# Optimization experiments

Measured on AMD Instinct MI355X. Metric: run time of the kernel, lower is better.

## Reference

```python
import jax, jax.numpy as jnp
import numpy as np

N = 50000       # num nodes
E = 800000      # num edges
F_NODE = 64     # node feature dim
F_EDGE = 16     # edge feature dim
HID = 32        # hidden_channels (per head)
HEADS = 4
HC = HEADS * HID  # 128
COND = 128      # condition_dim
NEG = 0.2       # GATv2 leaky_relu slope


def _lin(k, fi, fo):
    kw, kb = jax.random.split(k)
    s = 1.0 / np.sqrt(fi)
    W = jax.random.uniform(kw, (fi, fo), minval=-s, maxval=s, dtype=jnp.float32)
    b = jax.random.uniform(kb, (fo,), minval=-s, maxval=s, dtype=jnp.float32)
    return W, b


def setup_inputs() -> dict:
    key = jax.random.key(0)
    ks = jax.random.split(key, 16)
    x = jax.random.normal(ks[0], (N, F_NODE), dtype=jnp.float32)
    edge_index = jax.random.randint(ks[1], (2, E), 0, N)
    edge_attr = jax.random.normal(ks[2], (1, E, F_EDGE), dtype=jnp.float32)
    # conv1 params (GATv2Conv: lin_l, lin_r, lin_edge(no bias), att, out bias)
    w1l, b1l = _lin(ks[3], F_NODE, HC)
    w1r, b1r = _lin(ks[4], F_NODE, HC)
    w1e, _ = _lin(ks[5], F_EDGE, HC)
    att1 = jax.random.normal(ks[6], (HEADS, HID), dtype=jnp.float32) * 0.1
    bias1 = jnp.zeros((HC,), jnp.float32)
    # conv2 params
    w2l, b2l = _lin(ks[7], HC, HC)
    w2r, b2r = _lin(ks[8], HC, HC)
    w2e, _ = _lin(ks[9], F_EDGE, HC)
    att2 = jax.random.normal(ks[10], (HEADS, HID), dtype=jnp.float32) * 0.1
    bias2 = jnp.zeros((HC,), jnp.float32)
    # history_encoder
    hw, hb = _lin(ks[11], HC, COND)
    return dict(x=x, edge_index=edge_index, edge_attr=edge_attr,
                w1l=w1l, b1l=b1l, w1r=w1r, b1r=b1r, w1e=w1e, att1=att1, bias1=bias1,
                w2l=w2l, b2l=b2l, w2r=w2r, b2r=b2r, w2e=w2e, att2=att2, bias2=bias2,
                hw=hw, hb=hb)


def _gatv2(x, src, tgt, eattr, Wl, bl, Wr, br, We, att, bout):
    # x: [N, Fin]; src/tgt: [Ef]; eattr: [Ef, F_EDGE]
    xl = (x @ Wl + bl).reshape(-1, HEADS, HID)   # source transform
    xr = (x @ Wr + br).reshape(-1, HEADS, HID)   # target transform
    ee = (eattr @ We).reshape(-1, HEADS, HID)
    m = jax.nn.leaky_relu(xl[src] + xr[tgt] + ee, NEG)   # [Ef, H, C]
    logit = jnp.einsum('ehc,hc->eh', m, att)             # [Ef, H]
    # numerically-stable edge softmax over each target node's neighborhood
    mx = jax.ops.segment_max(logit, tgt, num_segments=N)
    p = jnp.exp(logit - mx[tgt])
    den = jax.ops.segment_sum(p, tgt, num_segments=N)
    alpha = p / den[tgt]                                 # [Ef, H]
    out = jax.ops.segment_sum(xl[src] * alpha[..., None], tgt, num_segments=N)
    return out.reshape(-1, HC) + bout                    # concat heads + bias


def reference(x, edge_index, edge_attr,
              w1l, b1l, w1r, b1r, w1e, att1, bias1,
              w2l, b2l, w2r, b2r, w2e, att2, bias2,
              hw, hb):
    ea = edge_attr[0]                      # edge_attr.squeeze(0)
    src, tgt = edge_index[0], edge_index[1]
    # add_self_loops with fill_value='mean': per-target mean of incoming edge_attr
    cnt = jax.ops.segment_sum(jnp.ones((E,), jnp.float32), tgt, num_segments=N)
    loop_attr = jax.ops.segment_sum(ea, tgt, num_segments=N) / jnp.maximum(cnt, 1.0)[:, None]
    loops = jnp.arange(N)
    src_f = jnp.concatenate([src, loops])
    tgt_f = jnp.concatenate([tgt, loops])
    ea_f = jnp.concatenate([ea, loop_attr], axis=0)
    h = jax.nn.relu(_gatv2(x, src_f, tgt_f, ea_f, w1l, b1l, w1r, b1r, w1e, att1, bias1))
    h = jax.nn.relu(_gatv2(h, src_f, tgt_f, ea_f, w2l, b2l, w2r, b2r, w2e, att2, bias2))
    h = h[None]                            # repeat to batch = edge_attr.size(0) = 1
    c = h @ hw + hb                        # history_encoder -> [1, N, COND]
    return c
```

## Files before the change

### kernel.cpp

```cpp
#include <hip/hip_runtime.h>
#include <hip/hip_bf16.h>
#include <math.h>

#define N_NODES 50000
#define N_EDGES 800000
#define NEG     0.2f

#define OFF_CNT    0
#define OFF_ROWPTR 50000
#define OFF_CURSOR 100000
#define OFF_PART   150000
#define OFF_CSRSE  150256
#define OFF_XL     1750272
#define OFF_XR     8150272

#define SCAN_BLOCKS 196
#define LNT 8

__global__ void hist_cnt_kernel(const int* __restrict__ tgt, int* __restrict__ cnt)
{
    int e = blockIdx.x * 256 + threadIdx.x;
    if (e >= N_EDGES) return;
    atomicAdd(&cnt[tgt[e]], 1);
}

__global__ void scanA_kernel(const int* __restrict__ cnt, int* __restrict__ rowptr,
                             int* __restrict__ part)
{
    __shared__ int s[256];
    int tid = threadIdx.x;
    int g = blockIdx.x * 256 + tid;
    int v = (g < N_NODES) ? cnt[g] : 0;
    s[tid] = v;
    __syncthreads();
    for (int off = 1; off < 256; off <<= 1) {
        int t = (tid >= off) ? s[tid - off] : 0;
        __syncthreads();
        s[tid] += t;
        __syncthreads();
    }
    if (g < N_NODES) rowptr[g] = s[tid] - v;
    if (tid == 255) part[blockIdx.x] = s[255];
}

__global__ void scanB_kernel(int* __restrict__ part)
{
    __shared__ int s[256];
    int tid = threadIdx.x;
    int v = (tid < SCAN_BLOCKS) ? part[tid] : 0;
    s[tid] = v;
    __syncthreads();
    for (int off = 1; off < 256; off <<= 1) {
        int t = (tid >= off) ? s[tid - off] : 0;
        __syncthreads();
        s[tid] += t;
        __syncthreads();
    }
    part[tid] = s[tid] - v;
}

__global__ void scanC_kernel(int* __restrict__ rowptr, const int* __restrict__ part,
                             int* __restrict__ cursor)
{
    int g = blockIdx.x * 256 + threadIdx.x;
    if (g >= N_NODES) return;
    int r = rowptr[g] + part[blockIdx.x];
    rowptr[g] = r;
    cursor[g] = r;
}

__global__ void scatter_kernel(const int* __restrict__ src, const int* __restrict__ tgt,
                               int* __restrict__ cursor, int2* __restrict__ csr_se)
{
    int e = blockIdx.x * 256 + threadIdx.x;
    if (e >= N_EDGES) return;
    int pos = atomicAdd(&cursor[tgt[e]], 1);
    csr_se[pos] = make_int2(src[e], e);
}

template<int K>
__global__ __launch_bounds__(128) void lin_kernel(const float* __restrict__ X,
    const float* __restrict__ Wl, const float* __restrict__ bl,
    const float* __restrict__ Wr, const float* __restrict__ br,
    float* __restrict__ xl, float* __restrict__ xr)
{
    __shared__ float s[LNT][K];
    int j = threadIdx.x;
    int nb = blockIdx.x * LNT;
    for (int t = 0; t < LNT; ++t) {
        int n = nb + t;
        if (n < N_NODES)
            for (int k = j; k < K; k += 128) s[t][k] = X[(size_t)n * K + k];
    }
    __syncthreads();
    float accL[LNT], accR[LNT];
    float blj = bl[j], brj = br[j];
    #pragma unroll
    for (int t = 0; t < LNT; ++t) { accL[t] = blj; accR[t] = brj; }
    for (int k = 0; k < K; ++k) {
        float wl = Wl[k * 128 + j], wr = Wr[k * 128 + j];
        #pragma unroll
        for (int t = 0; t < LNT; ++t) {
            accL[t] = fmaf(s[t][k], wl, accL[t]);
            accR[t] = fmaf(s[t][k], wr, accR[t]);
        }
    }
    for (int t = 0; t < LNT; ++t) {
        int n = nb + t;
        if (n < N_NODES) {
            xl[(size_t)n * 128 + j] = accL[t];
            xr[(size_t)n * 128 + j] = accR[t];
        }
    }
}

__global__ __launch_bounds__(256) void fused_kernel(
    const float* __restrict__ xl, const float* __restrict__ xr,
    const float* __restrict__ ea,
    const int2* __restrict__ csr_se, const int* __restrict__ rowptr,
    const int* __restrict__ cnt,
    const float* __restrict__ We, const float* __restrict__ att,
    const float* __restrict__ bias, float* __restrict__ out)
{
    __shared__ __align__(64) float sEa[4][4][16];
    int tid = threadIdx.x;
    int wave = tid >> 6, lane = tid & 63;
    int n = blockIdx.x * 4 + wave;
    if (n >= N_NODES) return;
    int c0 = lane * 2;
    int slot = lane >> 4, feat = lane & 15;

    float wreg0[16], wreg1[16];
    #pragma unroll
    for (int k = 0; k < 16; ++k) {
        float2 w2 = *(const float2*)(We + k * 128 + c0);
        wreg0[k] = w2.x; wreg1[k] = w2.y;
    }
    float a0 = att[c0], a1 = att[c0 + 1];

    int base = rowptr[n];
    int deg  = cnt[n];
    float2 xrt = *(const float2*)(xr + (size_t)n * 128 + c0);
    float2 xln = *(const float2*)(xl + (size_t)n * 128 + c0);

    float m = -INFINITY, den = 0.f, acc0 = 0.f, acc1 = 0.f;
    float eesum0 = 0.f, eesum1 = 0.f;

    int2 nse0 = make_int2(0, 0), nse1 = nse0, nse2 = nse0, nse3 = nse0;
    if (deg > 0) {
        nse0 = csr_se[base];     nse1 = csr_se[base + 1];
        nse2 = csr_se[base + 2]; nse3 = csr_se[base + 3];
    }
    for (int i = 0; i < deg; i += 4) {
        int2 se0 = nse0, se1 = nse1, se2 = nse2, se3 = nse3;
        bool v1 = (i + 1) < deg, v2 = (i + 2) < deg, v3 = (i + 3) < deg;
        int s0 = se0.x,           e0 = se0.y;
        int s1 = v1 ? se1.x : s0, e1 = v1 ? se1.y : e0;
        int s2 = v2 ? se2.x : s0, e2 = v2 ? se2.y : e0;
        int s3 = v3 ? se3.x : s0, e3 = v3 ? se3.y : e0;

        int es = (slot == 0) ? e0 : ((slot == 1) ? e1 : ((slot == 2) ? e2 : e3));
        sEa[wave][slot][feat] = ea[(size_t)es * 16 + feat];

        float2 x0 = *(const float2*)(xl + (size_t)s0 * 128 + c0);
        float2 x1 = *(const float2*)(xl + (size_t)s1 * 128 + c0);
        float2 x2 = *(const float2*)(xl + (size_t)s2 * 128 + c0);
        float2 x3 = *(const float2*)(xl + (size_t)s3 * 128 + c0);

        if (i + 4 < deg) {
            nse0 = csr_se[base + i + 4]; nse1 = csr_se[base + i + 5];
            nse2 = csr_se[base + i + 6]; nse3 = csr_se[base + i + 7];
        }

        float p0, p1, p2, p3;
#define EDGE_BODY(J, XJ, PJ, VJ)                                              \
        {                                                                     \
            const float4* er4 = (const float4*)&sEa[wave][J][0];              \
            float4 f0 = er4[0], f1 = er4[1], f2 = er4[2], f3 = er4[3];        \
            float t0 = f0.x * wreg0[0], t1 = f0.x * wreg1[0];                 \
            t0 = fmaf(f0.y, wreg0[1], t0);  t1 = fmaf(f0.y, wreg1[1], t1);    \
            t0 = fmaf(f0.z, wreg0[2], t0);  t1 = fmaf(f0.z, wreg1[2], t1);    \
            t0 = fmaf(f0.w, wreg0[3], t0);  t1 = fmaf(f0.w, wreg1[3], t1);    \
            t0 = fmaf(f1.x, wreg0[4], t0);  t1 = fmaf(f1.x, wreg1[4], t1);    \
            t0 = fmaf(f1.y, wreg0[5], t0);  t1 = fmaf(f1.y, wreg1[5], t1);    \
            t0 = fmaf(f1.z, wreg0[6], t0);  t1 = fmaf(f1.z, wreg1[6], t1);    \
            t0 = fmaf(f1.w, wreg0[7], t0);  t1 = fmaf(f1.w, wreg1[7], t1);    \
            t0 = fmaf(f2.x, wreg0[8], t0);  t1 = fmaf(f2.x, wreg1[8], t1);    \
            t0 = fmaf(f2.y, wreg0[9], t0);  t1 = fmaf(f2.y, wreg1[9], t1);    \
            t0 = fmaf(f2.z, wreg0[10], t0); t1 = fmaf(f2.z, wreg1[10], t1);   \
            t0 = fmaf(f2.w, wreg0[11], t0); t1 = fmaf(f2.w, wreg1[11], t1);   \
            t0 = fmaf(f3.x, wreg0[12], t0); t1 = fmaf(f3.x, wreg1[12], t1);   \
            t0 = fmaf(f3.y, wreg0[13], t0); t1 = fmaf(f3.y, wreg1[13], t1);   \
            t0 = fmaf(f3.z, wreg0[14], t0); t1 = fmaf(f3.z, wreg1[14], t1);   \
            t0 = fmaf(f3.w, wreg0[15], t0); t1 = fmaf(f3.w, wreg1[15], t1);   \
            eesum0 += (VJ) ? t0 : 0.f;      eesum1 += (VJ) ? t1 : 0.f;        \
            float q0 = XJ.x + xrt.x + t0;   q0 = (q0 > 0.f) ? q0 : NEG * q0;  \
            float q1 = XJ.y + xrt.y + t1;   q1 = (q1 > 0.f) ? q1 : NEG * q1;  \
            PJ = fmaf(q0, a0, q1 * a1);                                       \
        }
        EDGE_BODY(0, x0, p0, true)
        EDGE_BODY(1, x1, p1, v1)
        EDGE_BODY(2, x2, p2, v2)
        EDGE_BODY(3, x3, p3, v3)
#undef EDGE_BODY

        #pragma unroll
        for (int msk = 1; msk < 16; msk <<= 1) {
            p0 += __shfl_xor(p0, msk);
            p1 += __shfl_xor(p1, msk);
            p2 += __shfl_xor(p2, msk);
            p3 += __shfl_xor(p3, msk);
        }
        p1 = v1 ? p1 : -INFINITY;
        p2 = v2 ? p2 : -INFINITY;
        p3 = v3 ? p3 : -INFINITY;

        float nm = fmaxf(fmaxf(m, p0), fmaxf(fmaxf(p1, p2), p3));
        float sc = __expf(m - nm);
        float w0 = __expf(p0 - nm), w1 = __expf(p1 - nm);
        float w2 = __expf(p2 - nm), w3 = __expf(p3 - nm);
        den  = fmaf(den, sc, (w0 + w1) + (w2 + w3));
        acc0 = fmaf(acc0, sc, fmaf(w0, x0.x, fmaf(w1, x1.x, fmaf(w2, x2.x, w3 * x3.x))));
        acc1 = fmaf(acc1, sc, fmaf(w0, x0.y, fmaf(w1, x1.y, fmaf(w2, x2.y, w3 * x3.y))));
        m = nm;
    }

    {
        float rc = 1.0f / (float)(deg > 0 ? deg : 1);
        float ee0 = eesum0 * rc, ee1 = eesum1 * rc;
        float q0 = xln.x + xrt.x + ee0; q0 = (q0 > 0.f) ? q0 : NEG * q0;
        float q1 = xln.y + xrt.y + ee1; q1 = (q1 > 0.f) ? q1 : NEG * q1;
        float part = fmaf(q0, a0, q1 * a1);
        part += __shfl_xor(part, 1);
        part += __shfl_xor(part, 2);
        part += __shfl_xor(part, 4);
        part += __shfl_xor(part, 8);
        float nm = fmaxf(m, part);
        float sc = __expf(m - nm);
        float w  = __expf(part - nm);
        den  = fmaf(den, sc, w);
        acc0 = fmaf(acc0, sc, w * xln.x);
        acc1 = fmaf(acc1, sc, w * xln.y);
    }
    float rd = 1.0f / den;
    float o0 = fmaxf(fmaf(acc0, rd, bias[c0]), 0.f);
    float o1 = fmaxf(fmaf(acc1, rd, bias[c0 + 1]), 0.f);
    *(float2*)(out + (size_t)n * 128 + c0) = make_float2(o0, o1);
}

__global__ __launch_bounds__(128) void hist_kernel(float* __restrict__ io,
    const float* __restrict__ hw, const float* __restrict__ hb)
{
    __shared__ float s[LNT][128];
    int j = threadIdx.x;
    int nb = blockIdx.x * LNT;
    for (int t = 0; t < LNT; ++t) {
        int n = nb + t;
        if (n < N_NODES) s[t][j] = io[(size_t)n * 128 + j];
    }
    __syncthreads();
    float acc[LNT];
    float b = hb[j];
    #pragma unroll
    for (int t = 0; t < LNT; ++t) acc[t] = b;
    for (int k = 0; k < 128; ++k) {
        float w = hw[k * 128 + j];
        #pragma unroll
        for (int t = 0; t < LNT; ++t) acc[t] = fmaf(s[t][k], w, acc[t]);
    }
    for (int t = 0; t < LNT; ++t) {
        int n = nb + t;
        if (n < N_NODES) io[(size_t)n * 128 + j] = acc[t];
    }
}

extern "C" void kernel_launch(void* const* d_in, const int* in_sizes, int n_in,
                              void* d_out, int out_size, void* d_ws, size_t ws_size,
                              hipStream_t stream)
{
    const float* x    = (const float*)d_in[0];
    const int*   ei   = (const int*)d_in[1];
    const float* ea   = (const float*)d_in[2];
    const float* w1l  = (const float*)d_in[3];
    const float* b1l  = (const float*)d_in[4];
    const float* w1r  = (const float*)d_in[5];
    const float* b1r  = (const float*)d_in[6];
    const float* w1e  = (const float*)d_in[7];
    const float* att1 = (const float*)d_in[8];
    const float* bias1= (const float*)d_in[9];
    const float* w2l  = (const float*)d_in[10];
    const float* b2l  = (const float*)d_in[11];
    const float* w2r  = (const float*)d_in[12];
    const float* b2r  = (const float*)d_in[13];
    const float* w2e  = (const float*)d_in[14];
    const float* att2 = (const float*)d_in[15];
    const float* bias2= (const float*)d_in[16];
    const float* hw   = (const float*)d_in[17];
    const float* hb   = (const float*)d_in[18];
    const int* src = ei;
    const int* tgt = ei + N_EDGES;

    float* ws     = (float*)d_ws;
    int*   cnt    = (int*)(ws + OFF_CNT);
    int*   rowptr = (int*)(ws + OFF_ROWPTR);
    int*   cursor = (int*)(ws + OFF_CURSOR);
    int*   part   = (int*)(ws + OFF_PART);
    int2*  csr_se = (int2*)(ws + OFF_CSRSE);
    float* xl     = ws + OFF_XL;
    float* xr     = ws + OFF_XR;
    float* out    = (float*)d_out;

    hipMemsetAsync(cnt, 0, (size_t)N_NODES * 4, stream);

    hist_cnt_kernel<<<(N_EDGES + 255) / 256, 256, 0, stream>>>(tgt, cnt);
    scanA_kernel<<<SCAN_BLOCKS, 256, 0, stream>>>(cnt, rowptr, part);
    scanB_kernel<<<1, 256, 0, stream>>>(part);
    scanC_kernel<<<SCAN_BLOCKS, 256, 0, stream>>>(rowptr, part, cursor);
    scatter_kernel<<<(N_EDGES + 255) / 256, 256, 0, stream>>>(src, tgt, cursor, csr_se);

    lin_kernel<64><<<N_NODES / LNT, 128, 0, stream>>>(x, w1l, b1l, w1r, b1r, xl, xr);
    fused_kernel<<<(N_NODES + 3) / 4, 256, 0, stream>>>(
        xl, xr, ea, csr_se, rowptr, cnt, w1e, att1, bias1, out);

    lin_kernel<128><<<N_NODES / LNT, 128, 0, stream>>>(out, w2l, b2l, w2r, b2r, xl, xr);
    fused_kernel<<<(N_NODES + 3) / 4, 256, 0, stream>>>(
        xl, xr, ea, csr_se, rowptr, cnt, w2e, att2, bias2, out);

    hist_kernel<<<N_NODES / LNT, 128, 0, stream>>>(out, hw, hb);
}
```

Baseline: 659.1 us.

## Replace node linear kernels with register-tiled shared-memory GEMM

The per-layer lin kernels and the history-encoder kernel are replaced by one templated GEMM. It stages the whole weight matrix in LDS and computes 4x4 output tiles per thread with float4 loads, looping over 32-row tiles in a persistent grid of 1024 blocks. The aim is to stop re-reading weights from global memory for every small 8-node block and to raise arithmetic intensity. In exchange, the left and right projections are now separate launches that each read X again. The K=128 variant uses about 80KB of LDS per block, which may limit occupancy.

```diff
diff --git a/kernel.cpp b/kernel.cpp
--- a/kernel.cpp
+++ b/kernel.cpp
@@ -15,7 +15,6 @@
 #define OFF_XR     8150272
 
 #define SCAN_BLOCKS 196
-#define LNT 8
 
 __global__ void hist_cnt_kernel(const int* __restrict__ tgt, int* __restrict__ cnt)
 {
@@ -78,39 +77,50 @@
     csr_se[pos] = make_int2(src[e], e);
 }
 
-template<int K>
-__global__ __launch_bounds__(128) void lin_kernel(const float* __restrict__ X,
-    const float* __restrict__ Wl, const float* __restrict__ bl,
-    const float* __restrict__ Wr, const float* __restrict__ br,
-    float* __restrict__ xl, float* __restrict__ xr)
-{
-    __shared__ float s[LNT][K];
-    int j = threadIdx.x;
-    int nb = blockIdx.x * LNT;
-    for (int t = 0; t < LNT; ++t) {
-        int n = nb + t;
-        if (n < N_NODES)
-            for (int k = j; k < K; k += 128) s[t][k] = X[(size_t)n * K + k];
-    }
-    __syncthreads();
-    float accL[LNT], accR[LNT];
-    float blj = bl[j], brj = br[j];
-    #pragma unroll
-    for (int t = 0; t < LNT; ++t) { accL[t] = blj; accR[t] = brj; }
-    for (int k = 0; k < K; ++k) {
-        float wl = Wl[k * 128 + j], wr = Wr[k * 128 + j];
-        #pragma unroll
-        for (int t = 0; t < LNT; ++t) {
-            accL[t] = fmaf(s[t][k], wl, accL[t]);
-            accR[t] = fmaf(s[t][k], wr, accR[t]);
-        }
-    }
-    for (int t = 0; t < LNT; ++t) {
-        int n = nb + t;
-        if (n < N_NODES) {
-            xl[(size_t)n * 128 + j] = accL[t];
-            xr[(size_t)n * 128 + j] = accR[t];
-        }
+template<int KK>
+__global__ __launch_bounds__(256) void gemm_kernel(
+    const float* __restrict__ X, const float* __restrict__ W,
+    const float* __restrict__ bias, float* __restrict__ Y)
+{
+    __shared__ float sW[KK * 128];
+    __shared__ float sX[32 * KK];
+    int tid = threadIdx.x;
+    for (int idx = tid * 4; idx < KK * 128; idx += 1024)
+        *(float4*)&sW[idx] = *(const float4*)&W[idx];
+    int tc = (tid & 31) * 4;
+    int tn = (tid >> 5) * 4;
+    float4 b4 = *(const float4*)&bias[tc];
+
+    for (int tb = blockIdx.x * 32; tb < N_NODES; tb += gridDim.x * 32) {
+        __syncthreads();
+        for (int idx = tid * 4; idx < 32 * KK; idx += 1024) {
+            if (tb + idx / KK < N_NODES)
+                *(float4*)&sX[idx] = *(const float4*)&X[(size_t)tb * KK + idx];
+        }
+        __syncthreads();
+        float4 a0 = b4, a1 = b4, a2 = b4, a3 = b4;
+#define FMA4(A, S, Wv) A.x = fmaf(S, Wv.x, A.x); A.y = fmaf(S, Wv.y, A.y); \
+                       A.z = fmaf(S, Wv.z, A.z); A.w = fmaf(S, Wv.w, A.w);
+        for (int k = 0; k < KK; k += 4) {
+            float4 x0 = *(const float4*)&sX[(tn + 0) * KK + k];
+            float4 x1 = *(const float4*)&sX[(tn + 1) * KK + k];
+            float4 x2 = *(const float4*)&sX[(tn + 2) * KK + k];
+            float4 x3 = *(const float4*)&sX[(tn + 3) * KK + k];
+            float4 w0 = *(const float4*)&sW[(k + 0) * 128 + tc];
+            float4 w1 = *(const float4*)&sW[(k + 1) * 128 + tc];
+            float4 w2 = *(const float4*)&sW[(k + 2) * 128 + tc];
+            float4 w3 = *(const float4*)&sW[(k + 3) * 128 + tc];
+            FMA4(a0, x0.x, w0) FMA4(a0, x0.y, w1) FMA4(a0, x0.z, w2) FMA4(a0, x0.w, w3)
+            FMA4(a1, x1.x, w0) FMA4(a1, x1.y, w1) FMA4(a1, x1.z, w2) FMA4(a1, x1.w, w3)
+            FMA4(a2, x2.x, w0) FMA4(a2, x2.y, w1) FMA4(a2, x2.z, w2) FMA4(a2, x2.w, w3)
+            FMA4(a3, x3.x, w0) FMA4(a3, x3.y, w1) FMA4(a3, x3.z, w2) FMA4(a3, x3.w, w3)
+        }
+#undef FMA4
+        int n0 = tb + tn;
+        if (n0 + 0 < N_NODES) *(float4*)&Y[(size_t)(n0 + 0) * 128 + tc] = a0;
+        if (n0 + 1 < N_NODES) *(float4*)&Y[(size_t)(n0 + 1) * 128 + tc] = a1;
+        if (n0 + 2 < N_NODES) *(float4*)&Y[(size_t)(n0 + 2) * 128 + tc] = a2;
+        if (n0 + 3 < N_NODES) *(float4*)&Y[(size_t)(n0 + 3) * 128 + tc] = a3;
     }
 }
 
@@ -248,32 +258,6 @@
     *(float2*)(out + (size_t)n * 128 + c0) = make_float2(o0, o1);
 }
 
-__global__ __launch_bounds__(128) void hist_kernel(float* __restrict__ io,
-    const float* __restrict__ hw, const float* __restrict__ hb)
-{
-    __shared__ float s[LNT][128];
-    int j = threadIdx.x;
-    int nb = blockIdx.x * LNT;
-    for (int t = 0; t < LNT; ++t) {
-        int n = nb + t;
-        if (n < N_NODES) s[t][j] = io[(size_t)n * 128 + j];
-    }
-    __syncthreads();
-    float acc[LNT];
-    float b = hb[j];
-    #pragma unroll
-    for (int t = 0; t < LNT; ++t) acc[t] = b;
-    for (int k = 0; k < 128; ++k) {
-        float w = hw[k * 128 + j];
-        #pragma unroll
-        for (int t = 0; t < LNT; ++t) acc[t] = fmaf(s[t][k], w, acc[t]);
-    }
-    for (int t = 0; t < LNT; ++t) {
-        int n = nb + t;
-        if (n < N_NODES) io[(size_t)n * 128 + j] = acc[t];
-    }
-}
-
 extern "C" void kernel_launch(void* const* d_in, const int* in_sizes, int n_in,
                               void* d_out, int out_size, void* d_ws, size_t ws_size,
                               hipStream_t stream)
@@ -318,13 +302,15 @@
     scanC_kernel<<<SCAN_BLOCKS, 256, 0, stream>>>(rowptr, part, cursor);
     scatter_kernel<<<(N_EDGES + 255) / 256, 256, 0, stream>>>(src, tgt, cursor, csr_se);
 
-    lin_kernel<64><<<N_NODES / LNT, 128, 0, stream>>>(x, w1l, b1l, w1r, b1r, xl, xr);
+    gemm_kernel<64><<<1024, 256, 0, stream>>>(x, w1l, b1l, xl);
+    gemm_kernel<64><<<1024, 256, 0, stream>>>(x, w1r, b1r, xr);
     fused_kernel<<<(N_NODES + 3) / 4, 256, 0, stream>>>(
         xl, xr, ea, csr_se, rowptr, cnt, w1e, att1, bias1, out);
 
-    lin_kernel<128><<<N_NODES / LNT, 128, 0, stream>>>(out, w2l, b2l, w2r, b2r, xl, xr);
+    gemm_kernel<128><<<1024, 256, 0, stream>>>(out, w2l, b2l, xl);
+    gemm_kernel<128><<<1024, 256, 0, stream>>>(out, w2r, b2r, xr);
     fused_kernel<<<(N_NODES + 3) / 4, 256, 0, stream>>>(
         xl, xr, ea, csr_se, rowptr, cnt, w2e, att2, bias2, out);
 
-    hist_kernel<<<N_NODES / LNT, 128, 0, stream>>>(out, hw, hb);
-}
+    gemm_kernel<128><<<1024, 256, 0, stream>>>(out, hw, hb, out);
+}
```

After: 602.0 us. 1.09x faster.
